# Optimization experiments

Measured on AMD Instinct MI355X. Metric: run time of the kernel, lower is better.

Reference implementation:

```python
import jax, jax.numpy as jnp
import numpy as np

D_MODEL = 768
HEADS = 12
GROUPS = 2
DK = D_MODEL // HEADS  # 64
KV_DIM = DK * GROUPS   # 128


def setup_inputs() -> dict:
    key = jax.random.key(0)
    ks = jax.random.split(key, 11)
    bs, seq = 4, 2048
    sd = 0.02
    return {
        "q": jax.random.normal(ks[0], (bs, seq, D_MODEL), jnp.float32),
        "k": jax.random.normal(ks[1], (bs, seq, D_MODEL), jnp.float32),
        "v": jax.random.normal(ks[2], (bs, seq, D_MODEL), jnp.float32),
        "Wq": jax.random.normal(ks[3], (D_MODEL, D_MODEL), jnp.float32) * sd,
        "bq": jnp.zeros((D_MODEL,), jnp.float32),
        "Wk": jax.random.normal(ks[4], (D_MODEL, KV_DIM), jnp.float32) * sd,
        "bk": jnp.zeros((KV_DIM,), jnp.float32),
        "Wv": jax.random.normal(ks[5], (D_MODEL, KV_DIM), jnp.float32) * sd,
        "bv": jnp.zeros((KV_DIM,), jnp.float32),
        "Wo": jax.random.normal(ks[6], (D_MODEL, D_MODEL), jnp.float32) * sd,
        "bo": jnp.zeros((D_MODEL,), jnp.float32),
    }


def reference(q, k, v, Wq, bq, Wk, bk, Wv, bv, Wo, bo):
    bs, sq, _ = q.shape
    sk = k.shape[1]
    rep = HEADS // GROUPS

    # projections
    qp = (q @ Wq + bq).reshape(bs, sq, HEADS, DK).transpose(0, 2, 1, 3)  # [b,h,sq,dk]
    kp = (k @ Wk + bk).reshape(bs, sk, GROUPS, DK)
    vp = (v @ Wv + bv).reshape(bs, sk, GROUPS, DK)
    # torch .repeat on group axis tiles the groups (pattern g0,g1,g0,g1,...)
    kp = jnp.tile(kp, (1, 1, rep, 1)).transpose(0, 2, 1, 3)  # [b,h,sk,dk]
    vp = jnp.tile(vp, (1, 1, rep, 1)).transpose(0, 2, 1, 3)  # [b,h,sk,dk]

    # NOTE: original module never applies self.scale -> unscaled scores (faithful)
    score = jnp.einsum("bhqd,bhkd->bhqk", qp, kp)
    attn = jax.nn.softmax(score, axis=-1)  # dropout is identity at eval
    out = jnp.einsum("bhqk,bhkd->bhqd", attn, vp)
    out = out.transpose(0, 2, 1, 3).reshape(bs, sq, D_MODEL)
    return out @ Wo + bo
```

## Files before the change

### kernel.cpp

```cpp
#include <hip/hip_runtime.h>
#include <hip/hip_bf16.h>

typedef short v8s __attribute__((ext_vector_type(8)));
typedef short v4s __attribute__((ext_vector_type(4)));
typedef float v4f __attribute__((ext_vector_type(4)));

#define BS 4
#define SEQ 2048
#define DMODEL 768
#define HEADS 12
#define GROUPS 2
#define DK 64
#define LOG2E 1.4426950408889634f

static __device__ __forceinline__ short f2bs(float f) {
    __hip_bfloat16 h = __float2bfloat16(f);
    return *reinterpret_cast<short*>(&h);
}

static __device__ __forceinline__ float fast_exp2(float x) {
#if __has_builtin(__builtin_amdgcn_exp2f)
    return __builtin_amdgcn_exp2f(x);
#else
    return __expf(x * 0.6931471805599453f);
#endif
}

struct alignas(8) s4pack { short a, b, c, d; };

__global__ __launch_bounds__(256) void convert_q(
    const float* __restrict__ q, short* __restrict__ qbf)
{
    const size_t base = (size_t)blockIdx.x * 4096;
#pragma unroll
    for (int r = 0; r < 4; ++r) {
        const size_t i = base + r * 1024 + threadIdx.x * 4;
        const float4 a = *reinterpret_cast<const float4*>(q + i);
        s4pack p{f2bs(a.x), f2bs(a.y), f2bs(a.z), f2bs(a.w)};
        *reinterpret_cast<s4pack*>(qbf + i) = p;
    }
}

__global__ __launch_bounds__(256) void wtrans_all(
    const float* __restrict__ Wq, const float* __restrict__ Wk,
    const float* __restrict__ Wv, const float* __restrict__ Wo,
    short* __restrict__ WqT, short* __restrict__ WkT,
    short* __restrict__ WvT, short* __restrict__ WoT)
{
    const int z = blockIdx.z;
    const float* W;
    short* WT;
    int N;
    if (z == 0)      { W = Wq; WT = WqT; N = 768; }
    else if (z == 1) { W = Wo; WT = WoT; N = 768; }
    else if (z == 2) { W = Wk; WT = WkT; N = 128; }
    else             { W = Wv; WT = WvT; N = 128; }
    const int n0 = blockIdx.x * 32, k0 = blockIdx.y * 32;
    if (n0 >= N) return;

    __shared__ float t[32][33];
    const int lx = threadIdx.x & 31, ly = threadIdx.x >> 5;
#pragma unroll
    for (int r = 0; r < 4; ++r)
        t[ly + r * 8][lx] = W[(size_t)(k0 + ly + r * 8) * N + n0 + lx];
    __syncthreads();
#pragma unroll
    for (int r = 0; r < 4; ++r)
        WT[(size_t)(n0 + ly + r * 8) * DMODEL + k0 + lx] = f2bs(t[lx][ly + r * 8]);
}

__global__ __launch_bounds__(256) void proj_all(
    const short* __restrict__ qbf, const float* __restrict__ kin,
    const float* __restrict__ vin,
    const short* __restrict__ WqT, const short* __restrict__ WkT,
    const short* __restrict__ WvT,
    const float* __restrict__ bq, const float* __restrict__ bk,
    const float* __restrict__ bv,
    short* __restrict__ Qp, short* __restrict__ Kp, short* __restrict__ Vt)
{
    const int LS = 40;
    __shared__ short lA[64 * 40];
    __shared__ short lB[128 * 40];

    const int y = blockIdx.y;
    const short* WT = (y < 6) ? WqT + (size_t)y * 128 * DMODEL
                              : (y == 6) ? WkT : WvT;
    const float* bias = (y < 6) ? bq + y * 128 : (y == 6) ? bk : bv;

    const int tid  = threadIdx.x;
    const int lane = tid & 63;
    const int wid  = tid >> 6;
    const int l16  = lane & 15;
    const int quad = lane >> 4;
    const int wm   = wid & 1;
    const int wn   = wid >> 1;
    const int bm   = blockIdx.x;

    v4f acc[2][4];
#pragma unroll
    for (int i = 0; i < 2; ++i)
#pragma unroll
        for (int j = 0; j < 4; ++j) acc[i][j] = (v4f){0.f, 0.f, 0.f, 0.f};

    for (int kt = 0; kt < 24; ++kt) {
        const int k0 = kt * 32;
        if (y < 6) {
            const int row = tid >> 2, c8 = (tid & 3) << 3;
            *reinterpret_cast<v8s*>(&lA[row * LS + c8]) =
                *reinterpret_cast<const v8s*>(qbf + (size_t)(bm * 64 + row) * DMODEL + k0 + c8);
        } else {
            const float* A = (y == 6) ? kin : vin;
#pragma unroll
            for (int r = 0; r < 2; ++r) {
                int f4  = tid + 256 * r;
                int row = f4 >> 3;
                int c4  = (f4 & 7) << 2;
                const float4 a = *reinterpret_cast<const float4*>(
                    A + (size_t)(bm * 64 + row) * DMODEL + k0 + c4);
                s4pack p{f2bs(a.x), f2bs(a.y), f2bs(a.z), f2bs(a.w)};
                *reinterpret_cast<s4pack*>(&lA[row * LS + c4]) = p;
            }
        }
#pragma unroll
        for (int r = 0; r < 2; ++r) {
            int f8  = tid + 256 * r;
            int row = f8 >> 2;
            int c8  = (f8 & 3) << 3;
            *reinterpret_cast<v8s*>(&lB[row * LS + c8]) =
                *reinterpret_cast<const v8s*>(WT + (size_t)row * DMODEL + k0 + c8);
        }
        __syncthreads();

        v8s af[2], bf[4];
#pragma unroll
        for (int i = 0; i < 2; ++i)
            af[i] = *reinterpret_cast<const v8s*>(&lA[(wm * 32 + i * 16 + l16) * LS + quad * 8]);
#pragma unroll
        for (int j = 0; j < 4; ++j)
            bf[j] = *reinterpret_cast<const v8s*>(&lB[(wn * 64 + j * 16 + l16) * LS + quad * 8]);
#pragma unroll
        for (int i = 0; i < 2; ++i)
#pragma unroll
            for (int j = 0; j < 4; ++j)
                acc[i][j] = __builtin_amdgcn_mfma_f32_16x16x32_bf16(af[i], bf[j], acc[i][j], 0, 0, 0);
        __syncthreads();
    }

#pragma unroll
    for (int i = 0; i < 2; ++i) {
#pragma unroll
        for (int j = 0; j < 4; ++j) {
            const int Cl = wn * 64 + j * 16 + l16;
            const float bvv = bias[Cl];
#pragma unroll
            for (int reg = 0; reg < 4; ++reg) {
                const int R = bm * 64 + wm * 32 + i * 16 + quad * 4 + reg;
                const int b = R >> 11;
                const int s = R & 2047;
                if (y < 6) {
                    const int C = y * 128 + Cl;
                    const int h = C >> 6, d = C & 63;
                    Qp[((size_t)(b * HEADS + h) * SEQ + s) * DK + d] =
                        f2bs((acc[i][j][reg] + bvv) * LOG2E);
                } else if (y == 6) {
                    const int g = Cl >> 6, d = Cl & 63;
                    Kp[((size_t)(b * GROUPS + g) * SEQ + s) * DK + d] =
                        f2bs(acc[i][j][reg] + bvv);
                } else {
                    const int g = Cl >> 6, d = Cl & 63;
                    Vt[((size_t)(b * GROUPS + g) * DK + d) * SEQ + s] =
                        f2bs(acc[i][j][reg] + bvv);
                }
            }
        }
    }
}

__global__ __launch_bounds__(256) void attn_kernel(
    const short* __restrict__ Qp, const short* __restrict__ Kp,
    const short* __restrict__ Vt, short* __restrict__ Oat)
{
    const int LS = 72;
    __shared__ short lK[64 * 72];
    __shared__ short lV[64 * 72];

    const int qt = blockIdx.x, h = blockIdx.y, b = blockIdx.z;
    const int g = h & 1;
    const int tid  = threadIdx.x;
    const int lane = tid & 63;
    const int wid  = tid >> 6;
    const int l16  = lane & 15;
    const int quad = lane >> 4;

    v8s qf[2][2];
#pragma unroll
    for (int mi = 0; mi < 2; ++mi) {
        const size_t qbase =
            ((size_t)(b * HEADS + h) * SEQ + qt * 128 + wid * 32 + mi * 16 + l16) * DK;
        qf[mi][0] = *reinterpret_cast<const v8s*>(Qp + qbase + quad * 8);
        qf[mi][1] = *reinterpret_cast<const v8s*>(Qp + qbase + quad * 8 + 32);
    }

    const size_t kbase = (size_t)(b * GROUPS + g) * SEQ * DK;
    const size_t vbase = (size_t)(b * GROUPS + g) * DK * SEQ;

    const short one = (short)0x3F80;
    const v8s ones8 = {one, one, one, one, one, one, one, one};

    v4f oacc[2][5];
#pragma unroll
    for (int mi = 0; mi < 2; ++mi)
#pragma unroll
        for (int n = 0; n < 5; ++n) oacc[mi][n] = (v4f){0.f, 0.f, 0.f, 0.f};

    for (int kt = 0; kt < 32; ++kt) {
#pragma unroll
        for (int r = 0; r < 2; ++r) {
            int i8  = tid + 256 * r;
            int row = i8 >> 3;
            int c8  = (i8 & 7) << 3;
            *reinterpret_cast<v8s*>(&lK[row * LS + c8]) =
                *reinterpret_cast<const v8s*>(Kp + kbase + (size_t)(kt * 64 + row) * DK + c8);
            const v8s w = *reinterpret_cast<const v8s*>(
                Vt + vbase + (size_t)row * SEQ + kt * 64 + c8);
            const int a0 = c8, a1 = c8 + 4;
            const int ck0 = (a0 & 0x23) | ((a0 & 0x0C) << 1) | ((a0 & 0x10) >> 2);
            const int ck1 = (a1 & 0x23) | ((a1 & 0x0C) << 1) | ((a1 & 0x10) >> 2);
            s4pack lo{w[0], w[1], w[2], w[3]};
            s4pack hi{w[4], w[5], w[6], w[7]};
            *reinterpret_cast<s4pack*>(&lV[row * LS + ck0]) = lo;
            *reinterpret_cast<s4pack*>(&lV[row * LS + ck1]) = hi;
        }
        __syncthreads();

        v4s pp[2][4];
#pragma unroll
        for (int j = 0; j < 4; ++j) {
            const v8s kf0 = *reinterpret_cast<const v8s*>(&lK[(j * 16 + l16) * LS + quad * 8]);
            const v8s kf1 = *reinterpret_cast<const v8s*>(&lK[(j * 16 + l16) * LS + quad * 8 + 32]);
#pragma unroll
            for (int mi = 0; mi < 2; ++mi) {
                v4f z = (v4f){0.f, 0.f, 0.f, 0.f};
                z = __builtin_amdgcn_mfma_f32_16x16x32_bf16(kf0, qf[mi][0], z, 0, 0, 0);
                z = __builtin_amdgcn_mfma_f32_16x16x32_bf16(kf1, qf[mi][1], z, 0, 0, 0);
                v4s p;
#pragma unroll
                for (int reg = 0; reg < 4; ++reg) p[reg] = f2bs(fast_exp2(z[reg]));
                pp[mi][j] = p;
            }
        }

#pragma unroll
        for (int cj = 0; cj < 2; ++cj) {
            v8s pf[2];
#pragma unroll
            for (int mi = 0; mi < 2; ++mi)
                pf[mi] = __builtin_shufflevector(pp[mi][2 * cj], pp[mi][2 * cj + 1],
                                                 0, 1, 2, 3, 4, 5, 6, 7);
#pragma unroll
            for (int n = 0; n < 4; ++n) {
                const v8s vf = *reinterpret_cast<const v8s*>(
                    &lV[(n * 16 + l16) * LS + cj * 32 + quad * 8]);
#pragma unroll
                for (int mi = 0; mi < 2; ++mi)
                    oacc[mi][n] = __builtin_amdgcn_mfma_f32_16x16x32_bf16(pf[mi], vf, oacc[mi][n], 0, 0, 0);
            }
#pragma unroll
            for (int mi = 0; mi < 2; ++mi)
                oacc[mi][4] = __builtin_amdgcn_mfma_f32_16x16x32_bf16(pf[mi], ones8, oacc[mi][4], 0, 0, 0);
        }
        __syncthreads();
    }

#pragma unroll
    for (int mi = 0; mi < 2; ++mi) {
        float rdiv[4];
#pragma unroll
        for (int reg = 0; reg < 4; ++reg)
            rdiv[reg] = __builtin_amdgcn_rcpf(oacc[mi][4][reg]);
#pragma unroll
        for (int n = 0; n < 4; ++n)
#pragma unroll
            for (int reg = 0; reg < 4; ++reg) {
                const int qrow = qt * 128 + wid * 32 + mi * 16 + quad * 4 + reg;
                Oat[(size_t)(b * SEQ + qrow) * DMODEL + h * 64 + n * 16 + l16] =
                    f2bs(oacc[mi][n][reg] * rdiv[reg]);
            }
    }
}

__global__ __launch_bounds__(256) void out_gemm(
    const short* __restrict__ A, const short* __restrict__ WT,
    const float* __restrict__ bias, float* __restrict__ out)
{
    const int LS = 40;
    __shared__ short lA[64 * 40];
    __shared__ short lB[128 * 40];

    const int tid  = threadIdx.x;
    const int lane = tid & 63;
    const int wid  = tid >> 6;
    const int l16  = lane & 15;
    const int quad = lane >> 4;
    const int wm   = wid & 1;
    const int wn   = wid >> 1;
    const int bm   = blockIdx.x;
    const int bn   = blockIdx.y;

    v4f acc[2][4];
#pragma unroll
    for (int i = 0; i < 2; ++i)
#pragma unroll
        for (int j = 0; j < 4; ++j) acc[i][j] = (v4f){0.f, 0.f, 0.f, 0.f};

    for (int kt = 0; kt < 24; ++kt) {
        const int k0 = kt * 32;
        {
            const int row = tid >> 2, c8 = (tid & 3) << 3;
            *reinterpret_cast<v8s*>(&lA[row * LS + c8]) =
                *reinterpret_cast<const v8s*>(A + (size_t)(bm * 64 + row) * DMODEL + k0 + c8);
        }
#pragma unroll
        for (int r = 0; r < 2; ++r) {
            int f8  = tid + 256 * r;
            int row = f8 >> 2;
            int c8  = (f8 & 3) << 3;
            *reinterpret_cast<v8s*>(&lB[row * LS + c8]) =
                *reinterpret_cast<const v8s*>(WT + (size_t)(bn * 128 + row) * DMODEL + k0 + c8);
        }
        __syncthreads();

        v8s af[2], bf[4];
#pragma unroll
        for (int i = 0; i < 2; ++i)
            af[i] = *reinterpret_cast<const v8s*>(&lA[(wm * 32 + i * 16 + l16) * LS + quad * 8]);
#pragma unroll
        for (int j = 0; j < 4; ++j)
            bf[j] = *reinterpret_cast<const v8s*>(&lB[(wn * 64 + j * 16 + l16) * LS + quad * 8]);
#pragma unroll
        for (int i = 0; i < 2; ++i)
#pragma unroll
            for (int j = 0; j < 4; ++j)
                acc[i][j] = __builtin_amdgcn_mfma_f32_16x16x32_bf16(af[i], bf[j], acc[i][j], 0, 0, 0);
        __syncthreads();
    }

#pragma unroll
    for (int i = 0; i < 2; ++i)
#pragma unroll
        for (int j = 0; j < 4; ++j) {
            const int C = bn * 128 + wn * 64 + j * 16 + l16;
            const float bv = bias[C];
#pragma unroll
            for (int reg = 0; reg < 4; ++reg) {
                const int R = bm * 64 + wm * 32 + i * 16 + quad * 4 + reg;
                out[(size_t)R * DMODEL + C] = acc[i][j][reg] + bv;
            }
        }
}

extern "C" void kernel_launch(void* const* d_in, const int* in_sizes, int n_in,
                              void* d_out, int out_size, void* d_ws, size_t ws_size,
                              hipStream_t stream) {
    const float* q  = (const float*)d_in[0];
    const float* k  = (const float*)d_in[1];
    const float* v  = (const float*)d_in[2];
    const float* Wq = (const float*)d_in[3];
    const float* bq = (const float*)d_in[4];
    const float* Wk = (const float*)d_in[5];
    const float* bk = (const float*)d_in[6];
    const float* Wv = (const float*)d_in[7];
    const float* bv = (const float*)d_in[8];
    const float* Wo = (const float*)d_in[9];
    const float* bo = (const float*)d_in[10];

    short* WqT = (short*)d_ws;
    short* WkT = WqT + 589824;
    short* WvT = WkT + 98304;
    short* WoT = WvT + 98304;
    short* qbf = WoT + 589824;
    short* Qp  = qbf + 6291456;
    short* Kp  = Qp + (size_t)BS * HEADS * SEQ * DK;
    short* Vt  = Kp + (size_t)BS * GROUPS * SEQ * DK;
    short* Oat = Vt + (size_t)BS * GROUPS * SEQ * DK;

    convert_q<<<1536, 256, 0, stream>>>(q, qbf);
    wtrans_all<<<dim3(24, 24, 4), 256, 0, stream>>>(Wq, Wk, Wv, Wo, WqT, WkT, WvT, WoT);
    proj_all<<<dim3(128, 8), 256, 0, stream>>>(qbf, k, v, WqT, WkT, WvT,
                                               bq, bk, bv, Qp, Kp, Vt);
    attn_kernel<<<dim3(16, HEADS, BS), 256, 0, stream>>>(Qp, Kp, Vt, Oat);
    out_gemm<<<dim3(128, 6), 256, 0, stream>>>(Oat, WoT, bo, (float*)d_out);
}
```

Baseline: 259.2 us.

## Enlarge projection and attention tiles, pre-permute V in projection epilogue

```diff
diff --git a/kernel.cpp b/kernel.cpp
--- a/kernel.cpp
+++ b/kernel.cpp
@@ -79,7 +79,7 @@
     short* __restrict__ Qp, short* __restrict__ Kp, short* __restrict__ Vt)
 {
     const int LS = 40;
-    __shared__ short lA[64 * 40];
+    __shared__ short lA[128 * 40];
     __shared__ short lB[128 * 40];
 
     const int y = blockIdx.y;
@@ -96,50 +96,53 @@
     const int wn   = wid >> 1;
     const int bm   = blockIdx.x;
 
-    v4f acc[2][4];
-#pragma unroll
-    for (int i = 0; i < 2; ++i)
+    v4f acc[4][4];
+#pragma unroll
+    for (int i = 0; i < 4; ++i)
 #pragma unroll
         for (int j = 0; j < 4; ++j) acc[i][j] = (v4f){0.f, 0.f, 0.f, 0.f};
 
     for (int kt = 0; kt < 24; ++kt) {
         const int k0 = kt * 32;
         if (y < 6) {
-            const int row = tid >> 2, c8 = (tid & 3) << 3;
-            *reinterpret_cast<v8s*>(&lA[row * LS + c8]) =
-                *reinterpret_cast<const v8s*>(qbf + (size_t)(bm * 64 + row) * DMODEL + k0 + c8);
+#pragma unroll
+            for (int r = 0; r < 2; ++r) {
+                int idx = tid + 256 * r;
+                int row = idx >> 2, c8 = (idx & 3) << 3;
+                *reinterpret_cast<v8s*>(&lA[row * LS + c8]) =
+                    *reinterpret_cast<const v8s*>(qbf + (size_t)(bm * 128 + row) * DMODEL + k0 + c8);
+            }
         } else {
             const float* A = (y == 6) ? kin : vin;
 #pragma unroll
-            for (int r = 0; r < 2; ++r) {
+            for (int r = 0; r < 4; ++r) {
                 int f4  = tid + 256 * r;
                 int row = f4 >> 3;
                 int c4  = (f4 & 7) << 2;
                 const float4 a = *reinterpret_cast<const float4*>(
-                    A + (size_t)(bm * 64 + row) * DMODEL + k0 + c4);
+                    A + (size_t)(bm * 128 + row) * DMODEL + k0 + c4);
                 s4pack p{f2bs(a.x), f2bs(a.y), f2bs(a.z), f2bs(a.w)};
                 *reinterpret_cast<s4pack*>(&lA[row * LS + c4]) = p;
             }
         }
 #pragma unroll
         for (int r = 0; r < 2; ++r) {
-            int f8  = tid + 256 * r;
-            int row = f8 >> 2;
-            int c8  = (f8 & 3) << 3;
+            int idx = tid + 256 * r;
+            int row = idx >> 2, c8 = (idx & 3) << 3;
             *reinterpret_cast<v8s*>(&lB[row * LS + c8]) =
                 *reinterpret_cast<const v8s*>(WT + (size_t)row * DMODEL + k0 + c8);
         }
         __syncthreads();
 
-        v8s af[2], bf[4];
-#pragma unroll
-        for (int i = 0; i < 2; ++i)
-            af[i] = *reinterpret_cast<const v8s*>(&lA[(wm * 32 + i * 16 + l16) * LS + quad * 8]);
+        v8s af[4], bf[4];
+#pragma unroll
+        for (int i = 0; i < 4; ++i)
+            af[i] = *reinterpret_cast<const v8s*>(&lA[(wm * 64 + i * 16 + l16) * LS + quad * 8]);
 #pragma unroll
         for (int j = 0; j < 4; ++j)
             bf[j] = *reinterpret_cast<const v8s*>(&lB[(wn * 64 + j * 16 + l16) * LS + quad * 8]);
 #pragma unroll
-        for (int i = 0; i < 2; ++i)
+        for (int i = 0; i < 4; ++i)
 #pragma unroll
             for (int j = 0; j < 4; ++j)
                 acc[i][j] = __builtin_amdgcn_mfma_f32_16x16x32_bf16(af[i], bf[j], acc[i][j], 0, 0, 0);
@@ -147,14 +150,14 @@
     }
 
 #pragma unroll
-    for (int i = 0; i < 2; ++i) {
+    for (int i = 0; i < 4; ++i) {
 #pragma unroll
         for (int j = 0; j < 4; ++j) {
             const int Cl = wn * 64 + j * 16 + l16;
             const float bvv = bias[Cl];
 #pragma unroll
             for (int reg = 0; reg < 4; ++reg) {
-                const int R = bm * 64 + wm * 32 + i * 16 + quad * 4 + reg;
+                const int R = bm * 128 + wm * 64 + i * 16 + quad * 4 + reg;
                 const int b = R >> 11;
                 const int s = R & 2047;
                 if (y < 6) {
@@ -168,7 +171,8 @@
                         f2bs(acc[i][j][reg] + bvv);
                 } else {
                     const int g = Cl >> 6, d = Cl & 63;
-                    Vt[((size_t)(b * GROUPS + g) * DK + d) * SEQ + s] =
+                    const int s2 = (s & ~63) | (s & 0x23) | ((s & 0x0C) << 1) | ((s & 0x10) >> 2);
+                    Vt[((size_t)(b * GROUPS + g) * DK + d) * SEQ + s2] =
                         f2bs(acc[i][j][reg] + bvv);
                 }
             }
@@ -180,9 +184,10 @@
     const short* __restrict__ Qp, const short* __restrict__ Kp,
     const short* __restrict__ Vt, short* __restrict__ Oat)
 {
-    const int LS = 72;
-    __shared__ short lK[64 * 72];
-    __shared__ short lV[64 * 72];
+    const int LSK = 72;
+    const int LSV = 136;
+    __shared__ short lK[128 * 72];
+    __shared__ short lV[64 * 136];
 
     const int qt = blockIdx.x, h = blockIdx.y, b = blockIdx.z;
     const int g = h & 1;
@@ -213,61 +218,59 @@
 #pragma unroll
         for (int n = 0; n < 5; ++n) oacc[mi][n] = (v4f){0.f, 0.f, 0.f, 0.f};
 
-    for (int kt = 0; kt < 32; ++kt) {
-#pragma unroll
-        for (int r = 0; r < 2; ++r) {
-            int i8  = tid + 256 * r;
-            int row = i8 >> 3;
-            int c8  = (i8 & 7) << 3;
-            *reinterpret_cast<v8s*>(&lK[row * LS + c8]) =
-                *reinterpret_cast<const v8s*>(Kp + kbase + (size_t)(kt * 64 + row) * DK + c8);
-            const v8s w = *reinterpret_cast<const v8s*>(
-                Vt + vbase + (size_t)row * SEQ + kt * 64 + c8);
-            const int a0 = c8, a1 = c8 + 4;
-            const int ck0 = (a0 & 0x23) | ((a0 & 0x0C) << 1) | ((a0 & 0x10) >> 2);
-            const int ck1 = (a1 & 0x23) | ((a1 & 0x0C) << 1) | ((a1 & 0x10) >> 2);
-            s4pack lo{w[0], w[1], w[2], w[3]};
-            s4pack hi{w[4], w[5], w[6], w[7]};
-            *reinterpret_cast<s4pack*>(&lV[row * LS + ck0]) = lo;
-            *reinterpret_cast<s4pack*>(&lV[row * LS + ck1]) = hi;
-        }
-        __syncthreads();
-
-        v4s pp[2][4];
-#pragma unroll
-        for (int j = 0; j < 4; ++j) {
-            const v8s kf0 = *reinterpret_cast<const v8s*>(&lK[(j * 16 + l16) * LS + quad * 8]);
-            const v8s kf1 = *reinterpret_cast<const v8s*>(&lK[(j * 16 + l16) * LS + quad * 8 + 32]);
-#pragma unroll
-            for (int mi = 0; mi < 2; ++mi) {
-                v4f z = (v4f){0.f, 0.f, 0.f, 0.f};
-                z = __builtin_amdgcn_mfma_f32_16x16x32_bf16(kf0, qf[mi][0], z, 0, 0, 0);
-                z = __builtin_amdgcn_mfma_f32_16x16x32_bf16(kf1, qf[mi][1], z, 0, 0, 0);
-                v4s p;
-#pragma unroll
-                for (int reg = 0; reg < 4; ++reg) p[reg] = f2bs(fast_exp2(z[reg]));
-                pp[mi][j] = p;
-            }
-        }
-
-#pragma unroll
-        for (int cj = 0; cj < 2; ++cj) {
-            v8s pf[2];
-#pragma unroll
-            for (int mi = 0; mi < 2; ++mi)
-                pf[mi] = __builtin_shufflevector(pp[mi][2 * cj], pp[mi][2 * cj + 1],
-                                                 0, 1, 2, 3, 4, 5, 6, 7);
-#pragma unroll
-            for (int n = 0; n < 4; ++n) {
-                const v8s vf = *reinterpret_cast<const v8s*>(
-                    &lV[(n * 16 + l16) * LS + cj * 32 + quad * 8]);
+    for (int kt = 0; kt < 16; ++kt) {
+#pragma unroll
+        for (int r = 0; r < 4; ++r) {
+            const int idx = tid + 256 * r;
+            const int rowK = idx >> 3, cK = (idx & 7) << 3;
+            *reinterpret_cast<v8s*>(&lK[rowK * LSK + cK]) =
+                *reinterpret_cast<const v8s*>(Kp + kbase + (size_t)(kt * 128 + rowK) * DK + cK);
+            const int rowV = idx >> 4, cV = (idx & 15) << 3;
+            *reinterpret_cast<v8s*>(&lV[rowV * LSV + cV]) =
+                *reinterpret_cast<const v8s*>(Vt + vbase + (size_t)rowV * SEQ + kt * 128 + cV);
+        }
+        __syncthreads();
+
+#pragma unroll
+        for (int kt2 = 0; kt2 < 2; ++kt2) {
+            v4s pp[2][4];
+#pragma unroll
+            for (int j = 0; j < 4; ++j) {
+                const v8s kf0 = *reinterpret_cast<const v8s*>(
+                    &lK[(kt2 * 64 + j * 16 + l16) * LSK + quad * 8]);
+                const v8s kf1 = *reinterpret_cast<const v8s*>(
+                    &lK[(kt2 * 64 + j * 16 + l16) * LSK + quad * 8 + 32]);
+#pragma unroll
+                for (int mi = 0; mi < 2; ++mi) {
+                    v4f z = (v4f){0.f, 0.f, 0.f, 0.f};
+                    z = __builtin_amdgcn_mfma_f32_16x16x32_bf16(kf0, qf[mi][0], z, 0, 0, 0);
+                    z = __builtin_amdgcn_mfma_f32_16x16x32_bf16(kf1, qf[mi][1], z, 0, 0, 0);
+                    v4s p;
+#pragma unroll
+                    for (int reg = 0; reg < 4; ++reg) p[reg] = f2bs(fast_exp2(z[reg]));
+                    pp[mi][j] = p;
+                }
+            }
+
+#pragma unroll
+            for (int cj = 0; cj < 2; ++cj) {
+                v8s pf[2];
 #pragma unroll
                 for (int mi = 0; mi < 2; ++mi)
-                    oacc[mi][n] = __builtin_amdgcn_mfma_f32_16x16x32_bf16(pf[mi], vf, oacc[mi][n], 0, 0, 0);
-            }
-#pragma unroll
-            for (int mi = 0; mi < 2; ++mi)
-                oacc[mi][4] = __builtin_amdgcn_mfma_f32_16x16x32_bf16(pf[mi], ones8, oacc[mi][4], 0, 0, 0);
+                    pf[mi] = __builtin_shufflevector(pp[mi][2 * cj], pp[mi][2 * cj + 1],
+                                                     0, 1, 2, 3, 4, 5, 6, 7);
+#pragma unroll
+                for (int n = 0; n < 4; ++n) {
+                    const v8s vf = *reinterpret_cast<const v8s*>(
+                        &lV[(n * 16 + l16) * LSV + kt2 * 64 + cj * 32 + quad * 8]);
+#pragma unroll
+                    for (int mi = 0; mi < 2; ++mi)
+                        oacc[mi][n] = __builtin_amdgcn_mfma_f32_16x16x32_bf16(pf[mi], vf, oacc[mi][n], 0, 0, 0);
+                }
+#pragma unroll
+                for (int mi = 0; mi < 2; ++mi)
+                    oacc[mi][4] = __builtin_amdgcn_mfma_f32_16x16x32_bf16(pf[mi], ones8, oacc[mi][4], 0, 0, 0);
+            }
         }
         __syncthreads();
     }
@@ -322,9 +325,8 @@
         }
 #pragma unroll
         for (int r = 0; r < 2; ++r) {
-            int f8  = tid + 256 * r;
-            int row = f8 >> 2;
-            int c8  = (f8 & 3) << 3;
+            int idx = tid + 256 * r;
+            int row = idx >> 2, c8 = (idx & 3) << 3;
             *reinterpret_cast<v8s*>(&lB[row * LS + c8]) =
                 *reinterpret_cast<const v8s*>(WT + (size_t)(bn * 128 + row) * DMODEL + k0 + c8);
         }
@@ -386,8 +388,8 @@
 
     convert_q<<<1536, 256, 0, stream>>>(q, qbf);
     wtrans_all<<<dim3(24, 24, 4), 256, 0, stream>>>(Wq, Wk, Wv, Wo, WqT, WkT, WvT, WoT);
-    proj_all<<<dim3(128, 8), 256, 0, stream>>>(qbf, k, v, WqT, WkT, WvT,
-                                               bq, bk, bv, Qp, Kp, Vt);
+    proj_all<<<dim3(64, 8), 256, 0, stream>>>(qbf, k, v, WqT, WkT, WvT,
+                                              bq, bk, bv, Qp, Kp, Vt);
     attn_kernel<<<dim3(16, HEADS, BS), 256, 0, stream>>>(Qp, Kp, Vt, Oat);
     out_gemm<<<dim3(128, 6), 256, 0, stream>>>(Oat, WoT, bo, (float*)d_out);
 }
```

Result: slower. 268.9 us (+3.7%).
